# Kernel optimization log

Measured on AMD Instinct MI355X. Metric: run time of the kernel, lower is better.

The kernel has to match this reference:

```python
import jax, jax.numpy as jnp
import numpy as np
from math import sqrt

EPS = 1e-5


def _head_branch(x, W, b, a, g, be):
    # x: (B,C,T,F); W: (H,O,C); b: (H,O); a: (H,) PReLU; g,be: (H,1,O,1,F)
    y = jnp.einsum('bctf,hoc->hbotf', x, W) + b[:, None, :, None, None]
    y = jnp.where(y > 0, y, a[:, None, None, None, None] * y)  # PReLU
    mean = y.mean(axis=(2, 4), keepdims=True)                  # ChannelNorm over (C,F)
    var = y.var(axis=(2, 4), keepdims=True)
    return (y - mean) / jnp.sqrt(var + EPS) * g + be           # (H,B,O,T,F)


def _proj(x, W, b, a, g, be):
    # x: (B,C,T,F); W: (C,C); b: (C,); a: scalar; g,be: (1,C,1,F)
    y = jnp.einsum('bctf,oc->botf', x, W) + b[None, :, None, None]
    y = jnp.where(y > 0, y, a * y)
    mean = y.mean(axis=(1, 3), keepdims=True)
    var = y.var(axis=(1, 3), keepdims=True)
    return (y - mean) / jnp.sqrt(var + EPS) * g + be


def setup_inputs() -> dict:
    key = jax.random.key(0)
    ks = jax.random.split(key, 8)
    B, C, T, F, H, HID = 4, 64, 1024, 128, 4, 4
    CH = C // H
    x = jax.random.normal(ks[0], (B, C, T, F), dtype=jnp.float32)
    Wq = jax.random.normal(ks[1], (H, HID, C), dtype=jnp.float32) * 0.05
    Wk = jax.random.normal(ks[2], (H, HID, C), dtype=jnp.float32) * 0.05
    Wv = jax.random.normal(ks[3], (H, CH, C), dtype=jnp.float32) * 0.05
    Wp = jax.random.normal(ks[4], (C, C), dtype=jnp.float32) * 0.05
    return {
        'x': x,
        'Wq': Wq, 'bq': jnp.zeros((H, HID)), 'aq': jnp.full((H,), 0.25),
        'gq': jnp.ones((H, 1, HID, 1, F)), 'betaq': jnp.zeros((H, 1, HID, 1, F)),
        'Wk': Wk, 'bk': jnp.zeros((H, HID)), 'ak': jnp.full((H,), 0.25),
        'gk': jnp.ones((H, 1, HID, 1, F)), 'betak': jnp.zeros((H, 1, HID, 1, F)),
        'Wv': Wv, 'bv': jnp.zeros((H, CH)), 'av': jnp.full((H,), 0.25),
        'gv': jnp.ones((H, 1, CH, 1, F)), 'betav': jnp.zeros((H, 1, CH, 1, F)),
        'Wp': Wp, 'bp': jnp.zeros((C,)), 'ap': jnp.float32(0.25),
        'gp': jnp.ones((1, C, 1, F)), 'betap': jnp.zeros((1, C, 1, F)),
    }


def reference(x, Wq, bq, aq, gq, betaq, Wk, bk, ak, gk, betak,
              Wv, bv, av, gv, betav, Wp, bp, ap, gp, betap):
    B, C, T, F = x.shape
    H = Wq.shape[0]
    CH = C // H
    q = _head_branch(x, Wq, bq, aq, gq, betaq)   # (H,B,HID,T,F)
    k = _head_branch(x, Wk, bk, ak, gk, betak)   # (H,B,HID,T,F)
    v = _head_branch(x, Wv, bv, av, gv, betav)   # (H,B,CH,T,F)
    # cat(dim=0) head-major, transpose(1,2), flatten -> (H*B, T, O*F)
    qf = q.transpose(0, 1, 3, 2, 4).reshape(H * B, T, -1)
    kf = k.transpose(0, 1, 3, 2, 4).reshape(H * B, T, -1)
    vf = v.transpose(0, 1, 3, 2, 4).reshape(H * B, T, -1)
    scale = 1.0 / sqrt(qf.shape[-1])
    attn = jax.nn.softmax(jnp.einsum('nqd,nkd->nqk', qf, kf) * scale, axis=-1)
    out = jnp.einsum('nqk,nkd->nqd', attn, vf)   # (H*B, T, CH*F)
    # invert torch's view/transpose chain back to (B,C,T,F)
    out = out.reshape(H, B, T, CH, F).transpose(1, 0, 3, 2, 4).reshape(B, C, T, F)
    out = _proj(out, Wp, bp, ap, gp, betap)
    return out + x
```

## Files before the change

### kernel.cpp

```cpp
#include <hip/hip_runtime.h>
#include <hip/hip_bf16.h>

typedef __attribute__((ext_vector_type(4))) float f32x4;
typedef __attribute__((ext_vector_type(8))) short short8;

__device__ __forceinline__ float bf2f(unsigned short u){
  union { unsigned u32; float f; } v; v.u32 = ((unsigned)u) << 16; return v.f;
}
__device__ __forceinline__ unsigned short f2bf(float f){
  union { float f; unsigned u; } v; v.f = f;
  unsigned x = v.u;
  unsigned r = x + 0x7fffu + ((x >> 16) & 1u);
  return (unsigned short)(r >> 16);
}
__device__ __forceinline__ short8 pack8(f32x4 a, f32x4 b){
  short8 r;
  r[0]=(short)f2bf(a[0]); r[1]=(short)f2bf(a[1]);
  r[2]=(short)f2bf(a[2]); r[3]=(short)f2bf(a[3]);
  r[4]=(short)f2bf(b[0]); r[5]=(short)f2bf(b[1]);
  r[6]=(short)f2bf(b[2]); r[7]=(short)f2bf(b[3]);
  return r;
}

__device__ __forceinline__ void gload_lds16(const unsigned short* g, unsigned short* l) {
  __builtin_amdgcn_global_load_lds(
      (const __attribute__((address_space(1))) unsigned int*)g,
      (__attribute__((address_space(3))) unsigned int*)l, 16, 0, 0);
}

__global__ __launch_bounds__(256) void prep_kernel(
    const float* bq, const float* aq, const float* bk, const float* ak,
    const float* bv, const float* av, const float* Wp,
    float* ball, float* aall, float* Wps)
{
  int idx = blockIdx.x * 256 + threadIdx.x;
  if (idx < 96) {
    int j = idx;
    float b, a;
    if (j < 16)      { b = bq[j];      a = aq[j >> 2]; }
    else if (j < 32) { b = bk[j - 16]; a = ak[(j - 16) >> 2]; }
    else             { b = bv[j - 32]; a = av[(j - 32) >> 4]; }
    ball[j] = b; aall[j] = a;
  } else if (idx < 96 + 4096) {
    int r = idx - 96; int o = r >> 6, c = r & 63;
    Wps[c * 64 + o] = Wp[o * 64 + c];
  }
}

__global__ __launch_bounds__(256, 2) void qkv_mfma(
    const float* __restrict__ x,
    const float* __restrict__ Wq, const float* __restrict__ Wk,
    const float* __restrict__ Wv,
    const float* __restrict__ ball, const float* __restrict__ aall,
    const float* __restrict__ gq, const float* __restrict__ gk,
    const float* __restrict__ gv,
    const float* __restrict__ beq, const float* __restrict__ bek,
    const float* __restrict__ bev,
    unsigned short* __restrict__ qf, unsigned short* __restrict__ kf,
    unsigned short* __restrict__ vf)
{
  __shared__ unsigned short upool[256 * 64];
  __shared__ float partS[4][96], partQ[4][96];
  __shared__ float gm[2][12], gi[2][12];
  __shared__ float bias_l[96], a_l[96];

  int tid = threadIdx.x;
  int t0 = blockIdx.x * 2, b = blockIdx.y;
  int lane = tid & 63, wave = tid >> 6;
  int l15 = lane & 15, quad = lane >> 4;

  if (tid < 96) { bias_l[tid] = ball[tid]; a_l[tid] = aall[tid]; }

  const float* wsrc[6] = {
    Wq + l15 * 64, Wk + l15 * 64,
    Wv + l15 * 64, Wv + (16 + l15) * 64,
    Wv + (32 + l15) * 64, Wv + (48 + l15) * 64
  };
  short8 afr[6][2];
  #pragma unroll
  for (int mt = 0; mt < 6; mt++)
    #pragma unroll
    for (int ks = 0; ks < 2; ks++) {
      const float* p = wsrc[mt] + ks * 32 + quad * 8;
      afr[mt][ks] = pack8(*(const f32x4*)p, *(const f32x4*)(p + 4));
    }

  unsigned short* xl = upool;
  #pragma unroll
  for (int it = 0; it < 4; it++) {
    int item = it * 256 + tid;
    int cb = item >> 7;
    int np = item & 127;
    int n = np * 2;
    int tl = n >> 7, f = n & 127;
    const float* gp = x + ((long)(b * 64 + cb * 8) * 1024 + t0 + tl) * 128 + f;
    short8 lo, hi;
    #pragma unroll
    for (int w = 0; w < 8; w++) {
      float2 v = *(const float2*)(gp + (long)w * 131072);
      lo[w] = (short)f2bf(v.x);
      hi[w] = (short)f2bf(v.y);
    }
    int perm = cb ^ (np & 7);
    *(short8*)&xl[n * 64 + perm * 8]       = lo;
    *(short8*)&xl[(n + 1) * 64 + perm * 8] = hi;
  }
  __syncthreads();

  f32x4 acc[6][4];
  #pragma unroll
  for (int mt = 0; mt < 6; mt++)
    #pragma unroll
    for (int nt = 0; nt < 4; nt++)
      acc[mt][nt] = {0.f, 0.f, 0.f, 0.f};

  int nb = wave * 64;
  #pragma unroll
  for (int ks = 0; ks < 2; ks++)
    #pragma unroll
    for (int nt = 0; nt < 4; nt++) {
      int n = nb + nt * 16 + l15;
      int perm = (ks * 4 + quad) ^ ((n >> 1) & 7);
      short8 bfrag = *(const short8*)&xl[n * 64 + perm * 8];
      #pragma unroll
      for (int mt = 0; mt < 6; mt++)
        acc[mt][nt] = __builtin_amdgcn_mfma_f32_16x16x32_bf16(
            afr[mt][ks], bfrag, acc[mt][nt], 0, 0, 0);
    }

  #pragma unroll
  for (int mt = 0; mt < 6; mt++)
    #pragma unroll
    for (int r = 0; r < 4; r++) {
      int j = mt * 16 + quad * 4 + r;
      float bb = bias_l[j], aa = a_l[j];
      #pragma unroll
      for (int nt = 0; nt < 4; nt++) {
        float v = acc[mt][nt][r] + bb;
        acc[mt][nt][r] = v > 0.f ? v : aa * v;
      }
      float s  = acc[mt][0][r] + acc[mt][1][r] + acc[mt][2][r] + acc[mt][3][r];
      float q2 = acc[mt][0][r]*acc[mt][0][r] + acc[mt][1][r]*acc[mt][1][r]
               + acc[mt][2][r]*acc[mt][2][r] + acc[mt][3][r]*acc[mt][3][r];
      #pragma unroll
      for (int m = 1; m <= 8; m <<= 1) {
        s  += __shfl_xor(s,  m, 64);
        q2 += __shfl_xor(q2, m, 64);
      }
      if (l15 == 0) { partS[wave][j] = s; partQ[wave][j] = q2; }
    }
  __syncthreads();

  if (tid < 24) {
    int g = tid % 12, tl2 = tid / 12;
    int r0 = (g < 4) ? g * 4 : (g < 8) ? 16 + (g - 4) * 4 : 32 + (g - 8) * 16;
    int nr = (g < 8) ? 4 : 16;
    float S = 0.f, Q = 0.f;
    for (int w = tl2 * 2; w < tl2 * 2 + 2; w++)
      for (int r = 0; r < nr; r++) { S += partS[w][r0 + r]; Q += partQ[w][r0 + r]; }
    float cnt = (float)(nr * 128);
    float mean = S / cnt;
    float var = fmaxf(Q / cnt - mean * mean, 0.f);
    gm[tl2][g] = mean;
    gi[tl2][g] = rsqrtf(var + 1e-5f);
  }

  unsigned short* yl = upool;
  int ch = tid & 31, jrow = tid >> 5;

  #pragma unroll
  for (int half = 0; half < 2; half++) {
    int jbase = half * 48;
    #pragma unroll
    for (int mt3 = 0; mt3 < 3; mt3++) {
      int mt = half * 3 + mt3;
      #pragma unroll
      for (int nt = 0; nt < 4; nt++) {
        int n = nb + nt * 16 + l15;
        #pragma unroll
        for (int r = 0; r < 4; r++) {
          int jrel = mt3 * 16 + quad * 4 + r;
          yl[jrel * 264 + n] = f2bf(acc[mt][nt][r]);
        }
      }
    }
    __syncthreads();

    #pragma unroll
    for (int itj = 0; itj < 6; itj++) {
      int j = jbase + itj * 8 + jrow;
      int n0 = ch * 8;
      int tl3 = n0 >> 7, f = n0 & 127;
      short8 y8 = *(const short8*)&yl[(j - jbase) * 264 + n0];
      int g = (j < 16) ? (j >> 2) : (j < 32) ? 4 + ((j - 16) >> 2) : 8 + ((j - 32) >> 4);
      float mean = gm[tl3][g], inv = gi[tl3][g];
      const float *gsrc, *bsrc;
      int jo;
      unsigned short* dst;
      if (j < 16) {
        jo = j; gsrc = gq; bsrc = beq;
        int h = j >> 2, o = j & 3;
        dst = qf + (((long)(h * 4 + b) * 1024 + t0 + tl3) * 512 + o * 128 + f);
      } else if (j < 32) {
        jo = j - 16; gsrc = gk; bsrc = bek;
        int h = jo >> 2, o = jo & 3;
        dst = kf + (((long)(h * 4 + b) * 1024 + t0 + tl3) * 512 + o * 128 + f);
      } else {
        jo = j - 32; gsrc = gv; bsrc = bev;
        int h = jo >> 4, o = jo & 15;
        dst = vf + (((long)(h * 4 + b) * 1024 + t0 + tl3) * 2048 + o * 128 + f);
      }
      f32x4 g0 = *(const f32x4*)(gsrc + jo * 128 + f);
      f32x4 g1 = *(const f32x4*)(gsrc + jo * 128 + f + 4);
      f32x4 b0 = *(const f32x4*)(bsrc + jo * 128 + f);
      f32x4 b1 = *(const f32x4*)(bsrc + jo * 128 + f + 4);
      short8 o8;
      #pragma unroll
      for (int i = 0; i < 4; i++) {
        o8[i]     = (short)f2bf((bf2f((unsigned short)y8[i])     - mean) * inv * g0[i] + b0[i]);
        o8[i + 4] = (short)f2bf((bf2f((unsigned short)y8[i + 4]) - mean) * inv * g1[i] + b1[i]);
      }
      *(short8*)dst = o8;
    }
    if (half == 0) __syncthreads();
  }
}

__global__ __launch_bounds__(256) void transpose_v(
    const unsigned short* __restrict__ vf, unsigned short* __restrict__ vfT)
{
  __shared__ unsigned short tile[64][65];
  int n = blockIdx.z;
  int d0 = blockIdx.x * 64, t0 = blockIdx.y * 64;
  int tid = threadIdx.x;
  int cr = tid >> 4, cc = (tid & 15) * 4;

  const unsigned short* src = vf + ((long)n * 1024 + t0) * 2048 + d0;
  #pragma unroll
  for (int i = 0; i < 4; i++) {
    int r = cr + i * 16;
    ushort4 u = *(const ushort4*)(src + (long)r * 2048 + cc);
    tile[r][cc + 0] = u.x; tile[r][cc + 1] = u.y;
    tile[r][cc + 2] = u.z; tile[r][cc + 3] = u.w;
  }
  __syncthreads();
  unsigned short* dst = vfT + ((long)n * 2048 + d0) * 1024 + t0;
  #pragma unroll
  for (int i = 0; i < 4; i++) {
    int r = cr + i * 16;
    ushort4 u;
    u.x = tile[cc + 0][r]; u.y = tile[cc + 1][r];
    u.z = tile[cc + 2][r]; u.w = tile[cc + 3][r];
    *(ushort4*)(dst + (long)r * 1024 + cc) = u;
  }
}

__global__ __launch_bounds__(256) void gemm_bt(
    const unsigned short* __restrict__ A, const unsigned short* __restrict__ B,
    unsigned short* __restrict__ CbA, unsigned short* __restrict__ CbB,
    int M, int N, int K, long sA, long sB, long sC, float scale)
{
  __shared__ unsigned short smem[128 * 136];
  unsigned short* As = smem;
  unsigned short* Bs = smem + 128 * 64;
  int tid = threadIdx.x;

  int gx = gridDim.x, gy = gridDim.y;
  int bid = blockIdx.x + gx * (blockIdx.y + gy * blockIdx.z);
  int nwg = gx * gy * (int)gridDim.z;
  int cpx = nwg >> 3;
  int tile = (bid & 7) * cpx + (bid >> 3);
  int tx = tile % gx, trem = tile / gx;
  int ty = trem % gy, z = trem / gy;

  int m0 = ty * 128, n0 = tx * 128;
  const unsigned short* Ab = A + (long)z * sA + (long)m0 * K;
  const unsigned short* Bb = B + (long)z * sB + (long)n0 * K;
  int lane = tid & 63, wave = tid >> 6;
  int wm = (wave >> 1) * 64, wn = (wave & 1) * 64;
  int l15 = lane & 15, quad = lane >> 4;

  f32x4 acc[4][4];
  #pragma unroll
  for (int i = 0; i < 4; i++)
    #pragma unroll
    for (int j = 0; j < 4; j++) acc[i][j] = {0.f, 0.f, 0.f, 0.f};

  int srow8 = lane >> 3;
  int sck   = (lane & 7) ^ srow8;

  for (int k0 = 0; k0 < K; k0 += 64) {
    #pragma unroll
    for (int it = 0; it < 4; it++) {
      int R = it * 32 + wave * 8;
      int row = R + srow8;
      gload_lds16(Ab + (long)row * K + k0 + sck * 8, &As[R * 64]);
      gload_lds16(Bb + (long)row * K + k0 + sck * 8, &Bs[R * 64]);
    }
    __syncthreads();
    #pragma unroll
    for (int ks = 0; ks < 2; ks++) {
      short8 af[4], bfr[4];
      #pragma unroll
      for (int i = 0; i < 4; i++) {
        int row = wm + i * 16 + l15;
        af[i] = *(const short8*)&As[row * 64 + ((ks * 4 + quad) ^ (row & 7)) * 8];
      }
      #pragma unroll
      for (int j = 0; j < 4; j++) {
        int row = wn + j * 16 + l15;
        bfr[j] = *(const short8*)&Bs[row * 64 + ((ks * 4 + quad) ^ (row & 7)) * 8];
      }
      #pragma unroll
      for (int i = 0; i < 4; i++)
        #pragma unroll
        for (int j = 0; j < 4; j++)
          acc[i][j] = __builtin_amdgcn_mfma_f32_16x16x32_bf16(af[i], bfr[j], acc[i][j], 0, 0, 0);
    }
    __syncthreads();
  }

  #pragma unroll
  for (int i = 0; i < 4; i++)
    #pragma unroll
    for (int j = 0; j < 4; j++) {
      int row0 = wm + i * 16 + quad * 4;
      int col = wn + j * 16 + l15;
      #pragma unroll
      for (int r = 0; r < 4; r++)
        smem[(row0 + r) * 136 + col] = f2bf(acc[i][j][r] * scale);
    }
  __syncthreads();
  unsigned short* Cz = (z < 8) ? (CbA + (long)z * sC) : (CbB + (long)(z - 8) * sC);
  #pragma unroll
  for (int it = 0; it < 8; it++) {
    int chunk = it * 256 + tid;
    int row = chunk >> 4, c8 = (chunk & 15) * 8;
    *(short8*)(Cz + (long)(m0 + row) * N + n0 + c8) = *(const short8*)&smem[row * 136 + c8];
  }
}

__global__ __launch_bounds__(256) void softmax_kernel(unsigned short* __restrict__ P)
{
  __shared__ float red[4];
  __shared__ float bmax, bsum;
  int row = blockIdx.x, z = blockIdx.y, tid = threadIdx.x;
  unsigned short* p = P + ((long)z * 1024 + row) * 1024;
  ushort4 u = *(ushort4*)(p + tid * 4);
  float v0 = bf2f(u.x), v1 = bf2f(u.y), v2 = bf2f(u.z), v3 = bf2f(u.w);

  float m = fmaxf(fmaxf(v0, v1), fmaxf(v2, v3));
  #pragma unroll
  for (int s = 1; s <= 32; s <<= 1) m = fmaxf(m, __shfl_xor(m, s, 64));
  if ((tid & 63) == 0) red[tid >> 6] = m;
  __syncthreads();
  if (tid == 0) bmax = fmaxf(fmaxf(red[0], red[1]), fmaxf(red[2], red[3]));
  __syncthreads();
  m = bmax;

  float e0 = __expf(v0 - m), e1 = __expf(v1 - m), e2 = __expf(v2 - m), e3 = __expf(v3 - m);
  float s = e0 + e1 + e2 + e3;
  #pragma unroll
  for (int k = 1; k <= 32; k <<= 1) s += __shfl_xor(s, k, 64);
  if ((tid & 63) == 0) red[tid >> 6] = s;
  __syncthreads();
  if (tid == 0) bsum = red[0] + red[1] + red[2] + red[3];
  __syncthreads();
  float inv = 1.0f / bsum;

  u.x = f2bf(e0 * inv); u.y = f2bf(e1 * inv);
  u.z = f2bf(e2 * inv); u.w = f2bf(e3 * inv);
  *(ushort4*)(p + tid * 4) = u;
}

__global__ __launch_bounds__(256) void proj_kernel(
    float* __restrict__ io,
    const unsigned short* __restrict__ ofA, const unsigned short* __restrict__ ofB,
    const float* __restrict__ Wps,
    const float* __restrict__ bp, const float* __restrict__ ap,
    const float* __restrict__ gp, const float* __restrict__ bep,
    const float* __restrict__ x)
{
  __shared__ float xl[64 * 128];
  __shared__ float wl[64 * 64];
  __shared__ float redS[4], redQ[4];
  __shared__ float smean, sinv;

  int tid = threadIdx.x;
  int t = blockIdx.x, b = blockIdx.y;

  #pragma unroll
  for (int i = 0; i < 4; i++) {
    int chunk = i * 256 + tid;
    int h = chunk >> 8;
    int dvc = (chunk & 255) * 8;
    int z = h * 4 + b;
    const unsigned short* base =
        (z < 8) ? (ofA + (long)z * 2097152) : (ofB + (long)(z - 8) * 2097152);
    short8 v = *(const short8*)(base + (long)t * 2048 + dvc);
    int c = h * 16 + (dvc >> 7);
    int f = dvc & 127;
    #pragma unroll
    for (int e = 0; e < 8; e++) xl[c * 128 + f + e] = bf2f((unsigned short)v[e]);
  }
  #pragma unroll
  for (int i = 0; i < 4; i++) {
    int id = tid + i * 256;
    ((f32x4*)wl)[id] = ((const f32x4*)Wps)[id];
  }
  __syncthreads();

  int fblk = tid & 31, rblk = tid >> 5;
  int f0 = fblk * 4, r0 = rblk * 8;

  float acc[8][4];
  #pragma unroll
  for (int rr = 0; rr < 8; rr++)
    #pragma unroll
    for (int ff = 0; ff < 4; ff++) acc[rr][ff] = 0.f;

  for (int c = 0; c < 64; c++) {
    f32x4 xv = *(const f32x4*)&xl[c * 128 + f0];
    f32x4 w0 = *(const f32x4*)&wl[c * 64 + r0];
    f32x4 w1 = *(const f32x4*)&wl[c * 64 + r0 + 4];
    #pragma unroll
    for (int rr = 0; rr < 4; rr++) {
      #pragma unroll
      for (int ff = 0; ff < 4; ff++) {
        acc[rr][ff]     += w0[rr] * xv[ff];
        acc[rr + 4][ff] += w1[rr] * xv[ff];
      }
    }
  }

  float aval = ap[0];
  #pragma unroll
  for (int rr = 0; rr < 8; rr++) {
    float bb = bp[r0 + rr];
    #pragma unroll
    for (int ff = 0; ff < 4; ff++) {
      float v = acc[rr][ff] + bb;
      acc[rr][ff] = v > 0.f ? v : aval * v;
    }
  }

  float s = 0.f, sq = 0.f;
  #pragma unroll
  for (int rr = 0; rr < 8; rr++)
    #pragma unroll
    for (int ff = 0; ff < 4; ff++) { s += acc[rr][ff]; sq += acc[rr][ff] * acc[rr][ff]; }
  #pragma unroll
  for (int m = 1; m <= 32; m <<= 1) { s += __shfl_xor(s, m, 64); sq += __shfl_xor(sq, m, 64); }
  if ((tid & 63) == 0) { redS[tid >> 6] = s; redQ[tid >> 6] = sq; }
  __syncthreads();
  if (tid == 0) {
    float S = redS[0] + redS[1] + redS[2] + redS[3];
    float Q = redQ[0] + redQ[1] + redQ[2] + redQ[3];
    float mean = S / 8192.0f;
    float var = fmaxf(Q / 8192.0f - mean * mean, 0.f);
    smean = mean; sinv = rsqrtf(var + 1e-5f);
  }
  __syncthreads();
  float mean = smean, inv = sinv;

  const float* xb = x + ((long)(b * 64) * 1024 + t) * 128;
  #pragma unroll
  for (int rr = 0; rr < 8; rr++) {
    int c = r0 + rr;
    f32x4 g4 = *(const f32x4*)(gp + c * 128 + f0);
    f32x4 b4 = *(const f32x4*)(bep + c * 128 + f0);
    f32x4 x4 = *(const f32x4*)(xb + (long)c * 131072 + f0);
    f32x4 o;
    o[0] = (acc[rr][0] - mean) * inv * g4[0] + b4[0] + x4[0];
    o[1] = (acc[rr][1] - mean) * inv * g4[1] + b4[1] + x4[1];
    o[2] = (acc[rr][2] - mean) * inv * g4[2] + b4[2] + x4[2];
    o[3] = (acc[rr][3] - mean) * inv * g4[3] + b4[3] + x4[3];
    *(f32x4*)(io + ((long)(b * 64 + c) * 1024 + t) * 128 + f0) = o;
  }
}

extern "C" void kernel_launch(void* const* d_in, const int* in_sizes, int n_in,
                              void* d_out, int out_size, void* d_ws, size_t ws_size,
                              hipStream_t stream)
{
  const float* x   = (const float*)d_in[0];
  const float* Wq  = (const float*)d_in[1];
  const float* bq  = (const float*)d_in[2];
  const float* aq  = (const float*)d_in[3];
  const float* gq  = (const float*)d_in[4];
  const float* beq = (const float*)d_in[5];
  const float* Wk  = (const float*)d_in[6];
  const float* bk  = (const float*)d_in[7];
  const float* ak  = (const float*)d_in[8];
  const float* gk  = (const float*)d_in[9];
  const float* bek = (const float*)d_in[10];
  const float* Wv  = (const float*)d_in[11];
  const float* bv  = (const float*)d_in[12];
  const float* av  = (const float*)d_in[13];
  const float* gv  = (const float*)d_in[14];
  const float* bev = (const float*)d_in[15];
  const float* Wp  = (const float*)d_in[16];
  const float* bp  = (const float*)d_in[17];
  const float* ap  = (const float*)d_in[18];
  const float* gp  = (const float*)d_in[19];
  const float* bep = (const float*)d_in[20];
  float* out = (float*)d_out;

  char* ws = (char*)d_ws;
  size_t off = 0;
  auto alloc = [&](size_t n) { size_t o = off; off += (n + 255) & ~(size_t)255; return o; };

  float* ball = (float*)(ws + alloc(96 * 4));
  float* aall = (float*)(ws + alloc(96 * 4));
  float* Wps  = (float*)(ws + alloc(4096 * 4));
  unsigned short* qf  = (unsigned short*)(ws + alloc((size_t)16 * 1024 * 512 * 2));
  unsigned short* kf  = (unsigned short*)(ws + alloc((size_t)16 * 1024 * 512 * 2));
  unsigned short* vf  = (unsigned short*)(ws + alloc((size_t)16 * 1024 * 2048 * 2));
  unsigned short* vfT = (unsigned short*)(ws + alloc((size_t)16 * 1024 * 2048 * 2));
  unsigned short* P   = vf;
  unsigned short* ofA = qf;
  unsigned short* ofB = (unsigned short*)((char*)vf + (size_t)32 * 1024 * 1024);

  prep_kernel<<<17, 256, 0, stream>>>(bq, aq, bk, ak, bv, av, Wp,
                                      ball, aall, Wps);

  qkv_mfma<<<dim3(512, 4), 256, 0, stream>>>(
      x, Wq, Wk, Wv, ball, aall, gq, gk, gv, beq, bek, bev, qf, kf, vf);

  transpose_v<<<dim3(32, 16, 16), 256, 0, stream>>>(vf, vfT);

  gemm_bt<<<dim3(8, 8, 16), 256, 0, stream>>>(
      qf, kf, P, P + (long)8 * 1024 * 1024, 1024, 1024, 512,
      (long)1024 * 512, (long)1024 * 512, (long)1024 * 1024,
      0.04419417382f );

  softmax_kernel<<<dim3(1024, 16), 256, 0, stream>>>(P);

  gemm_bt<<<dim3(16, 8, 16), 256, 0, stream>>>(
      P, vfT, ofA, ofB, 1024, 2048, 1024,
      (long)1024 * 1024, (long)2048 * 1024, (long)1024 * 2048, 1.0f);

  proj_kernel<<<dim3(1024, 4), 256, 0, stream>>>(out, ofA, ofB, Wps, bp, ap, gp, bep, x);
}
```

Before: 522.2 us.

## Split QKV projection to one timestep per block and pre-convert weights to bf16

The QKV kernel now handles one time step per block instead of two, doubling the grid. The four waves are arranged as a 2x2 grid over output rows and columns, so each wave holds half the accumulators and the launch bound allows three blocks per SM. Weights, gamma and beta are converted to bf16 once in the prep kernel, so each block loads smaller, pre-packed fragments instead of converting fp32 per block. In exchange, gamma and beta are rounded to bf16 and each block reads less x data per launch.

```diff
diff --git a/kernel.cpp b/kernel.cpp
--- a/kernel.cpp
+++ b/kernel.cpp
@@ -13,14 +13,6 @@
   unsigned r = x + 0x7fffu + ((x >> 16) & 1u);
   return (unsigned short)(r >> 16);
 }
-__device__ __forceinline__ short8 pack8(f32x4 a, f32x4 b){
-  short8 r;
-  r[0]=(short)f2bf(a[0]); r[1]=(short)f2bf(a[1]);
-  r[2]=(short)f2bf(a[2]); r[3]=(short)f2bf(a[3]);
-  r[4]=(short)f2bf(b[0]); r[5]=(short)f2bf(b[1]);
-  r[6]=(short)f2bf(b[2]); r[7]=(short)f2bf(b[3]);
-  return r;
-}
 
 __device__ __forceinline__ void gload_lds16(const unsigned short* g, unsigned short* l) {
   __builtin_amdgcn_global_load_lds(
@@ -31,7 +23,11 @@
 __global__ __launch_bounds__(256) void prep_kernel(
     const float* bq, const float* aq, const float* bk, const float* ak,
     const float* bv, const float* av, const float* Wp,
-    float* ball, float* aall, float* Wps)
+    const float* Wq, const float* Wk, const float* Wv,
+    const float* gq, const float* gk, const float* gv,
+    const float* beq, const float* bek, const float* bev,
+    float* ball, float* aall, float* Wps,
+    unsigned short* Wbf, unsigned short* gba, unsigned short* bba)
 {
   int idx = blockIdx.x * 256 + threadIdx.x;
   if (idx < 96) {
@@ -41,59 +37,65 @@
     else if (j < 32) { b = bk[j - 16]; a = ak[(j - 16) >> 2]; }
     else             { b = bv[j - 32]; a = av[(j - 32) >> 4]; }
     ball[j] = b; aall[j] = a;
-  } else if (idx < 96 + 4096) {
+  } else if (idx < 4192) {
     int r = idx - 96; int o = r >> 6, c = r & 63;
     Wps[c * 64 + o] = Wp[o * 64 + c];
-  }
-}
-
-__global__ __launch_bounds__(256, 2) void qkv_mfma(
+  } else if (idx < 10336) {
+    int r = idx - 4192; int j = r >> 6, c = r & 63;
+    float w = (j < 16) ? Wq[j * 64 + c] : (j < 32) ? Wk[(j - 16) * 64 + c]
+                                                   : Wv[(j - 32) * 64 + c];
+    Wbf[j * 64 + c] = f2bf(w);
+  } else if (idx < 22624) {
+    int r = idx - 10336; int j = r >> 7, f = r & 127;
+    float g = (j < 16) ? gq[j * 128 + f] : (j < 32) ? gk[(j - 16) * 128 + f]
+                                                    : gv[(j - 32) * 128 + f];
+    gba[j * 128 + f] = f2bf(g);
+  } else if (idx < 34912) {
+    int r = idx - 22624; int j = r >> 7, f = r & 127;
+    float be = (j < 16) ? beq[j * 128 + f] : (j < 32) ? bek[(j - 16) * 128 + f]
+                                                      : bev[(j - 32) * 128 + f];
+    bba[j * 128 + f] = f2bf(be);
+  }
+}
+
+__global__ __launch_bounds__(256, 3) void qkv_mfma(
     const float* __restrict__ x,
-    const float* __restrict__ Wq, const float* __restrict__ Wk,
-    const float* __restrict__ Wv,
+    const unsigned short* __restrict__ Wbf,
     const float* __restrict__ ball, const float* __restrict__ aall,
-    const float* __restrict__ gq, const float* __restrict__ gk,
-    const float* __restrict__ gv,
-    const float* __restrict__ beq, const float* __restrict__ bek,
-    const float* __restrict__ bev,
+    const unsigned short* __restrict__ gba, const unsigned short* __restrict__ bba,
     unsigned short* __restrict__ qf, unsigned short* __restrict__ kf,
     unsigned short* __restrict__ vf)
 {
-  __shared__ unsigned short upool[256 * 64];
+  __shared__ unsigned short upool[128 * 64];
   __shared__ float partS[4][96], partQ[4][96];
-  __shared__ float gm[2][12], gi[2][12];
+  __shared__ float gm[12], gi[12];
   __shared__ float bias_l[96], a_l[96];
 
   int tid = threadIdx.x;
-  int t0 = blockIdx.x * 2, b = blockIdx.y;
+  int t = blockIdx.x, b = blockIdx.y;
   int lane = tid & 63, wave = tid >> 6;
   int l15 = lane & 15, quad = lane >> 4;
+  int rowg = wave >> 1, colg = wave & 1;
 
   if (tid < 96) { bias_l[tid] = ball[tid]; a_l[tid] = aall[tid]; }
 
-  const float* wsrc[6] = {
-    Wq + l15 * 64, Wk + l15 * 64,
-    Wv + l15 * 64, Wv + (16 + l15) * 64,
-    Wv + (32 + l15) * 64, Wv + (48 + l15) * 64
-  };
-  short8 afr[6][2];
-  #pragma unroll
-  for (int mt = 0; mt < 6; mt++)
-    #pragma unroll
-    for (int ks = 0; ks < 2; ks++) {
-      const float* p = wsrc[mt] + ks * 32 + quad * 8;
-      afr[mt][ks] = pack8(*(const f32x4*)p, *(const f32x4*)(p + 4));
-    }
+  short8 afr[3][2];
+  #pragma unroll
+  for (int mt3 = 0; mt3 < 3; mt3++) {
+    int row = (rowg * 3 + mt3) * 16 + l15;
+    #pragma unroll
+    for (int ks = 0; ks < 2; ks++)
+      afr[mt3][ks] = *(const short8*)(Wbf + row * 64 + ks * 32 + quad * 8);
+  }
 
   unsigned short* xl = upool;
   #pragma unroll
-  for (int it = 0; it < 4; it++) {
+  for (int it = 0; it < 2; it++) {
     int item = it * 256 + tid;
-    int cb = item >> 7;
-    int np = item & 127;
+    int cb = item >> 6;
+    int np = item & 63;
     int n = np * 2;
-    int tl = n >> 7, f = n & 127;
-    const float* gp = x + ((long)(b * 64 + cb * 8) * 1024 + t0 + tl) * 128 + f;
+    const float* gp = x + ((long)(b * 64 + cb * 8) * 1024 + t) * 128 + n;
     short8 lo, hi;
     #pragma unroll
     for (int w = 0; w < 8; w++) {
@@ -107,14 +109,14 @@
   }
   __syncthreads();
 
-  f32x4 acc[6][4];
-  #pragma unroll
-  for (int mt = 0; mt < 6; mt++)
+  f32x4 acc[3][4];
+  #pragma unroll
+  for (int mt3 = 0; mt3 < 3; mt3++)
     #pragma unroll
     for (int nt = 0; nt < 4; nt++)
-      acc[mt][nt] = {0.f, 0.f, 0.f, 0.f};
-
-  int nb = wave * 64;
+      acc[mt3][nt] = {0.f, 0.f, 0.f, 0.f};
+
+  int nb = colg * 64;
   #pragma unroll
   for (int ks = 0; ks < 2; ks++)
     #pragma unroll
@@ -123,25 +125,25 @@
       int perm = (ks * 4 + quad) ^ ((n >> 1) & 7);
       short8 bfrag = *(const short8*)&xl[n * 64 + perm * 8];
       #pragma unroll
-      for (int mt = 0; mt < 6; mt++)
-        acc[mt][nt] = __builtin_amdgcn_mfma_f32_16x16x32_bf16(
-            afr[mt][ks], bfrag, acc[mt][nt], 0, 0, 0);
-    }
-
-  #pragma unroll
-  for (int mt = 0; mt < 6; mt++)
+      for (int mt3 = 0; mt3 < 3; mt3++)
+        acc[mt3][nt] = __builtin_amdgcn_mfma_f32_16x16x32_bf16(
+            afr[mt3][ks], bfrag, acc[mt3][nt], 0, 0, 0);
+    }
+
+  #pragma unroll
+  for (int mt3 = 0; mt3 < 3; mt3++)
     #pragma unroll
     for (int r = 0; r < 4; r++) {
-      int j = mt * 16 + quad * 4 + r;
+      int j = (rowg * 3 + mt3) * 16 + quad * 4 + r;
       float bb = bias_l[j], aa = a_l[j];
       #pragma unroll
       for (int nt = 0; nt < 4; nt++) {
-        float v = acc[mt][nt][r] + bb;
-        acc[mt][nt][r] = v > 0.f ? v : aa * v;
+        float v = acc[mt3][nt][r] + bb;
+        acc[mt3][nt][r] = v > 0.f ? v : aa * v;
       }
-      float s  = acc[mt][0][r] + acc[mt][1][r] + acc[mt][2][r] + acc[mt][3][r];
-      float q2 = acc[mt][0][r]*acc[mt][0][r] + acc[mt][1][r]*acc[mt][1][r]
-               + acc[mt][2][r]*acc[mt][2][r] + acc[mt][3][r]*acc[mt][3][r];
+      float s  = acc[mt3][0][r] + acc[mt3][1][r] + acc[mt3][2][r] + acc[mt3][3][r];
+      float q2 = acc[mt3][0][r]*acc[mt3][0][r] + acc[mt3][1][r]*acc[mt3][1][r]
+               + acc[mt3][2][r]*acc[mt3][2][r] + acc[mt3][3][r]*acc[mt3][3][r];
       #pragma unroll
       for (int m = 1; m <= 8; m <<= 1) {
         s  += __shfl_xor(s,  m, 64);
@@ -151,75 +153,67 @@
     }
   __syncthreads();
 
-  if (tid < 24) {
-    int g = tid % 12, tl2 = tid / 12;
+  if (tid < 12) {
+    int g = tid;
     int r0 = (g < 4) ? g * 4 : (g < 8) ? 16 + (g - 4) * 4 : 32 + (g - 8) * 16;
     int nr = (g < 8) ? 4 : 16;
+    int rw = (r0 < 48) ? 0 : 2;
     float S = 0.f, Q = 0.f;
-    for (int w = tl2 * 2; w < tl2 * 2 + 2; w++)
-      for (int r = 0; r < nr; r++) { S += partS[w][r0 + r]; Q += partQ[w][r0 + r]; }
+    for (int w2 = 0; w2 < 2; w2++)
+      for (int r = 0; r < nr; r++) { S += partS[rw + w2][r0 + r]; Q += partQ[rw + w2][r0 + r]; }
     float cnt = (float)(nr * 128);
     float mean = S / cnt;
     float var = fmaxf(Q / cnt - mean * mean, 0.f);
-    gm[tl2][g] = mean;
-    gi[tl2][g] = rsqrtf(var + 1e-5f);
+    gm[g] = mean;
+    gi[g] = rsqrtf(var + 1e-5f);
   }
 
   unsigned short* yl = upool;
-  int ch = tid & 31, jrow = tid >> 5;
+  int ch = tid & 15, jrow = tid >> 4;
 
   #pragma unroll
   for (int half = 0; half < 2; half++) {
-    int jbase = half * 48;
-    #pragma unroll
-    for (int mt3 = 0; mt3 < 3; mt3++) {
-      int mt = half * 3 + mt3;
-      #pragma unroll
-      for (int nt = 0; nt < 4; nt++) {
-        int n = nb + nt * 16 + l15;
+    if (rowg == half) {
+      #pragma unroll
+      for (int mt3 = 0; mt3 < 3; mt3++)
         #pragma unroll
-        for (int r = 0; r < 4; r++) {
-          int jrel = mt3 * 16 + quad * 4 + r;
-          yl[jrel * 264 + n] = f2bf(acc[mt][nt][r]);
+        for (int nt = 0; nt < 4; nt++) {
+          int n = nb + nt * 16 + l15;
+          #pragma unroll
+          for (int r = 0; r < 4; r++) {
+            int jrel = mt3 * 16 + quad * 4 + r;
+            yl[jrel * 136 + n] = f2bf(acc[mt3][nt][r]);
+          }
         }
-      }
     }
     __syncthreads();
 
     #pragma unroll
-    for (int itj = 0; itj < 6; itj++) {
-      int j = jbase + itj * 8 + jrow;
-      int n0 = ch * 8;
-      int tl3 = n0 >> 7, f = n0 & 127;
-      short8 y8 = *(const short8*)&yl[(j - jbase) * 264 + n0];
+    for (int itj = 0; itj < 3; itj++) {
+      int jrel = itj * 16 + jrow;
+      int j = half * 48 + jrel;
+      int f = ch * 8;
+      short8 y8 = *(const short8*)&yl[jrel * 136 + f];
       int g = (j < 16) ? (j >> 2) : (j < 32) ? 4 + ((j - 16) >> 2) : 8 + ((j - 32) >> 4);
-      float mean = gm[tl3][g], inv = gi[tl3][g];
-      const float *gsrc, *bsrc;
-      int jo;
+      float mean = gm[g], inv = gi[g];
       unsigned short* dst;
       if (j < 16) {
-        jo = j; gsrc = gq; bsrc = beq;
         int h = j >> 2, o = j & 3;
-        dst = qf + (((long)(h * 4 + b) * 1024 + t0 + tl3) * 512 + o * 128 + f);
+        dst = qf + (((long)(h * 4 + b) * 1024 + t) * 512 + o * 128 + f);
       } else if (j < 32) {
-        jo = j - 16; gsrc = gk; bsrc = bek;
-        int h = jo >> 2, o = jo & 3;
-        dst = kf + (((long)(h * 4 + b) * 1024 + t0 + tl3) * 512 + o * 128 + f);
+        int jo = j - 16; int h = jo >> 2, o = jo & 3;
+        dst = kf + (((long)(h * 4 + b) * 1024 + t) * 512 + o * 128 + f);
       } else {
-        jo = j - 32; gsrc = gv; bsrc = bev;
-        int h = jo >> 4, o = jo & 15;
-        dst = vf + (((long)(h * 4 + b) * 1024 + t0 + tl3) * 2048 + o * 128 + f);
+        int jo = j - 32; int h = jo >> 4, o = jo & 15;
+        dst = vf + (((long)(h * 4 + b) * 1024 + t) * 2048 + o * 128 + f);
       }
-      f32x4 g0 = *(const f32x4*)(gsrc + jo * 128 + f);
-      f32x4 g1 = *(const f32x4*)(gsrc + jo * 128 + f + 4);
-      f32x4 b0 = *(const f32x4*)(bsrc + jo * 128 + f);
-      f32x4 b1 = *(const f32x4*)(bsrc + jo * 128 + f + 4);
+      short8 g8 = *(const short8*)(gba + j * 128 + f);
+      short8 b8 = *(const short8*)(bba + j * 128 + f);
       short8 o8;
       #pragma unroll
-      for (int i = 0; i < 4; i++) {
-        o8[i]     = (short)f2bf((bf2f((unsigned short)y8[i])     - mean) * inv * g0[i] + b0[i]);
-        o8[i + 4] = (short)f2bf((bf2f((unsigned short)y8[i + 4]) - mean) * inv * g1[i] + b1[i]);
-      }
+      for (int i = 0; i < 8; i++)
+        o8[i] = (short)f2bf((bf2f((unsigned short)y8[i]) - mean) * inv
+                            * bf2f((unsigned short)g8[i]) + bf2f((unsigned short)b8[i]));
       *(short8*)dst = o8;
     }
     if (half == 0) __syncthreads();
@@ -513,6 +507,9 @@
   float* ball = (float*)(ws + alloc(96 * 4));
   float* aall = (float*)(ws + alloc(96 * 4));
   float* Wps  = (float*)(ws + alloc(4096 * 4));
+  unsigned short* Wbf = (unsigned short*)(ws + alloc(6144 * 2));
+  unsigned short* gba = (unsigned short*)(ws + alloc(12288 * 2));
+  unsigned short* bba = (unsigned short*)(ws + alloc(12288 * 2));
   unsigned short* qf  = (unsigned short*)(ws + alloc((size_t)16 * 1024 * 512 * 2));
   unsigned short* kf  = (unsigned short*)(ws + alloc((size_t)16 * 1024 * 512 * 2));
   unsigned short* vf  = (unsigned short*)(ws + alloc((size_t)16 * 1024 * 2048 * 2));
@@ -521,11 +518,12 @@
   unsigned short* ofA = qf;
   unsigned short* ofB = (unsigned short*)((char*)vf + (size_t)32 * 1024 * 1024);
 
-  prep_kernel<<<17, 256, 0, stream>>>(bq, aq, bk, ak, bv, av, Wp,
-                                      ball, aall, Wps);
-
-  qkv_mfma<<<dim3(512, 4), 256, 0, stream>>>(
-      x, Wq, Wk, Wv, ball, aall, gq, gk, gv, beq, bek, bev, qf, kf, vf);
+  prep_kernel<<<137, 256, 0, stream>>>(bq, aq, bk, ak, bv, av, Wp,
+                                       Wq, Wk, Wv, gq, gk, gv, beq, bek, bev,
+                                       ball, aall, Wps, Wbf, gba, bba);
+
+  qkv_mfma<<<dim3(1024, 4), 256, 0, stream>>>(
+      x, Wbf, ball, aall, gba, bba, qf, kf, vf);
 
   transpose_v<<<dim3(32, 16, 16), 256, 0, stream>>>(vf, vfT);
 
```

New measurement: 517.9 us. No clear change (-0.8%).
